# Kernel tuning notes

Measured on AMD Instinct MI355X. Metric: run time of the kernel, lower is better.

The kernel has to match this reference:

```python
import jax, jax.numpy as jnp
import numpy as np

DIM = 96
HEADS = 8
HH = 128
WW = 128
L = HH * WW
K = 256
B = 2


def setup_inputs() -> dict:
    key = jax.random.key(0)
    ks = jax.random.split(key, 8)
    s = 0.02
    return {
        "x": jax.random.normal(ks[0], (B, L, DIM), jnp.float32),
        "Wqkv": jax.random.normal(ks[1], (DIM, 3 * DIM), jnp.float32) * s,
        "W0": jax.random.normal(ks[2], (DIM, DIM), jnp.float32) * s,
        "E": jax.random.normal(ks[3], (L, K), jnp.float32) * s,
        "conv0_w": jax.random.normal(ks[4], (DIM, 1, 5, 5), jnp.float32) * s,
        "conv0_b": jnp.zeros((DIM,), jnp.float32),
        "conv_sp_w": jax.random.normal(ks[5], (DIM, 1, 7, 7), jnp.float32) * s,
        "conv_sp_b": jnp.zeros((DIM,), jnp.float32),
        "conv1_w": jax.random.normal(ks[6], (DIM, DIM, 1, 1), jnp.float32) * s,
        "conv1_b": jnp.zeros((DIM,), jnp.float32),
        "H": HH,
        "W": WW,
    }


def _conv(x, w, b, pad, dil, groups):
    y = jax.lax.conv_general_dilated(
        x, w, window_strides=(1, 1), padding=[(pad, pad), (pad, pad)],
        rhs_dilation=(dil, dil),
        dimension_numbers=("NCHW", "OIHW", "NCHW"),
        feature_group_count=groups)
    return y + b[None, :, None, None]


def _cnn_atten(x, H, W, conv0_w, conv0_b, conv_sp_w, conv_sp_b, conv1_w, conv1_b):
    # VAN-style Large-Kernel-Attention: dw5x5 -> dw7x7(dil=3) -> 1x1, gate by identity
    Bx, Lx, C = x.shape
    xi = x.reshape(Bx, H, W, C).transpose(0, 3, 1, 2)  # B,C,H,W
    a = _conv(xi, conv0_w, conv0_b, 2, 1, C)
    a = _conv(a, conv_sp_w, conv_sp_b, 9, 3, C)
    a = _conv(a, conv1_w, conv1_b, 0, 1, 1)
    out = xi * a
    return out.transpose(0, 2, 3, 1).reshape(Bx, Lx, C)


def reference(x, Wqkv, W0, E, conv0_w, conv0_b, conv_sp_w, conv_sp_b, conv1_w, conv1_b, H, W):
    Bx, Lx, C = x.shape
    dh = C // HEADS
    scale = dh ** (-0.5)
    qkv = (x @ Wqkv).reshape(Bx, Lx, 3, HEADS, dh).transpose(2, 0, 3, 1, 4)  # 3,B,h,L,d
    q, k, v = qkv[0], qkv[1], qkv[2]
    ca = _cnn_atten(x, H, W, conv0_w, conv0_b, conv_sp_w, conv_sp_b, conv1_w, conv1_b)  # B,L,C
    vf = v.transpose(0, 2, 1, 3).reshape(Bx, Lx, C)
    vf = ca * vf  # elementwise CNN gating of V
    v = vf.reshape(Bx, Lx, HEADS, dh).transpose(0, 2, 1, 3)  # B,h,L,d
    # Linformer-style sequence reduction: L -> K
    v = jnp.einsum("bhjd,jk->bhkd", v, E)
    k = jnp.einsum("bhjd,jk->bhkd", k, E)
    attn = jax.nn.softmax(jnp.einsum("bhid,bhkd->bhik", q, k) * scale, axis=-1)  # B,h,L,K
    o = jnp.einsum("bhik,bhkd->bhid", attn, v)
    o = o.transpose(0, 2, 1, 3).reshape(Bx, Lx, C)
    return o @ W0
```

## Files before the change

kernel.cpp:

```cpp
#include <hip/hip_runtime.h>

#define HH_ 128
#define WW_ 128
#define LL_ (HH_*WW_)
#define NH 8
#define DHD 12
#define KD 256
#define BB_ 2
#define NROW (BB_*LL_)

typedef __attribute__((ext_vector_type(8))) short short8v;
typedef __attribute__((ext_vector_type(4))) float f32x4;
typedef unsigned short ushortT;

__device__ __forceinline__ float4 ld4(const float* p) {
    return *reinterpret_cast<const float4*>(p);
}
__device__ __forceinline__ unsigned int pk2(float a, float b) {
    unsigned int ua = __float_as_uint(a);
    unsigned int ub = __float_as_uint(b);
    ua = (ua + 0x7FFFu + ((ua >> 16) & 1u)) >> 16;
    ub = (ub + 0x7FFFu + ((ub >> 16) & 1u)) >> 16;
    return ua | (ub << 16);
}
__device__ __forceinline__ ushortT bf1(float a) {
    unsigned int u = __float_as_uint(a);
    return (ushortT)((u + 0x7FFFu + ((u >> 16) & 1u)) >> 16);
}
__device__ __forceinline__ float ubf(ushortT v) {
    return __uint_as_float(((unsigned int)v) << 16);
}
__device__ __forceinline__ unsigned int cvtpk(float a, float b) {
    unsigned int r;
    asm("v_cvt_pk_bf16_f32 %0, %1, %2" : "=v"(r) : "v"(a), "v"(b));
    return r;
}

__global__ __launch_bounds__(256) void k_front(const float* __restrict__ x,
        const float* __restrict__ c0w, const float* __restrict__ c0b,
        const float* __restrict__ E, const float* __restrict__ Wq,
        const float* __restrict__ W0, const float* __restrict__ w1,
        float* __restrict__ a1, ushortT* __restrict__ ET,
        ushortT* __restrict__ wqT, ushortT* __restrict__ w0T,
        ushortT* __restrict__ w1c) {
    __shared__ __align__(16) float shf[2400];
    const int tid = threadIdx.x;
    if (blockIdx.x < 1024) {
        float* wl = shf;
        for (int i = tid; i < 25*96; i += 256) {
            int c = i / 25, t = i % 25;
            wl[t*96 + c] = c0w[i];
        }
        __syncthreads();
        const int c4 = (tid & 7)*4;
        const int px = tid >> 3;
        const int pix0 = blockIdx.x * 32;
        const int b = pix0 >> 14;
        const int y = (pix0 & 16383) >> 7;
        const int xx = (pix0 & 127) + px;
        float4 acc[3];
#pragma unroll
        for (int ch = 0; ch < 3; ++ch) { acc[ch].x=0.f; acc[ch].y=0.f; acc[ch].z=0.f; acc[ch].w=0.f; }
#pragma unroll
        for (int iy = 0; iy < 5; ++iy) {
            int y2 = y + iy - 2;
            if (y2 < 0 || y2 >= HH_) continue;
#pragma unroll
            for (int ix = 0; ix < 5; ++ix) {
                int x2 = xx + ix - 2;
                if (x2 < 0 || x2 >= WW_) continue;
                const float* src = x + ((b << 14) + y2*WW_ + x2)*96;
                const float* wt = &wl[(iy*5 + ix)*96];
#pragma unroll
                for (int ch = 0; ch < 3; ++ch) {
                    float4 xv = ld4(src + ch*32 + c4);
                    float4 wv = ld4(wt + ch*32 + c4);
                    acc[ch].x = fmaf(xv.x, wv.x, acc[ch].x);
                    acc[ch].y = fmaf(xv.y, wv.y, acc[ch].y);
                    acc[ch].z = fmaf(xv.z, wv.z, acc[ch].z);
                    acc[ch].w = fmaf(xv.w, wv.w, acc[ch].w);
                }
            }
        }
        float* dst = a1 + (long)(pix0 + px)*96;
#pragma unroll
        for (int ch = 0; ch < 3; ++ch) {
            float4 bv = ld4(c0b + ch*32 + c4);
            float4 r;
            r.x = acc[ch].x + bv.x; r.y = acc[ch].y + bv.y;
            r.z = acc[ch].z + bv.z; r.w = acc[ch].w + bv.w;
            *reinterpret_cast<float4*>(dst + ch*32 + c4) = r;
        }
    } else if (blockIdx.x < 2048) {
        ushortT* Tz = (ushortT*)shf;
        const int bid = blockIdx.x - 1024;
        const int jt = bid >> 2, kt = bid & 3;
        const int j0 = jt * 64, kk0 = kt * 64;
        for (int i = tid; i < 64*16; i += 256) {
            int row = i >> 4, s4 = (i & 15) << 2;
            float4 e4 = ld4(&E[(long)(j0 + row)*256 + kk0 + s4]);
            Tz[(s4 + 0)*66 + row] = bf1(e4.x);
            Tz[(s4 + 1)*66 + row] = bf1(e4.y);
            Tz[(s4 + 2)*66 + row] = bf1(e4.z);
            Tz[(s4 + 3)*66 + row] = bf1(e4.w);
        }
        __syncthreads();
        unsigned int* Tu = (unsigned int*)Tz;
        for (int i = tid; i < 64*32; i += 256) {
            int kk = i >> 5, s = i & 31;
            ((unsigned int*)ET)[(((long)(kk0 + kk) << 14) + j0 >> 1) + s] = Tu[kk*33 + s];
        }
    } else {
        int i = (blockIdx.x - 2048)*256 + tid;
        if (i < 27648) {
            int n = i / 96, k = i % 96;
            wqT[n*96 + k] = bf1(Wq[k*288 + n]);
        } else if (i < 36864) {
            int j = i - 27648;
            int n = j / 96, k = j % 96;
            w0T[n*96 + k] = bf1(W0[k*96 + n]);
        } else if (i < 46080) {
            int j = i - 36864;
            w1c[j] = bf1(w1[j]);
        }
    }
}

__global__ __launch_bounds__(256) void k_mid(const float* __restrict__ x,
        const ushortT* __restrict__ wqT, ushortT* __restrict__ qkv16,
        const float* __restrict__ a1, const float* __restrict__ cspw,
        const float* __restrict__ cspb, ushortT* __restrict__ a2_16) {
    __shared__ __align__(16) float shm[4704];
    const int tid = threadIdx.x;
    if (blockIdx.x < 512) {
        ushortT* xb = (ushortT*)shm;
        const int r0w = blockIdx.x * 64;
        for (int i = tid; i < 64*48; i += 256) {
            int r = i / 48, cp = i % 48;
            const float* sp = x + (long)(r0w + r)*96 + cp*2;
            ((unsigned int*)xb)[r*52 + cp] = pk2(sp[0], sp[1]);
        }
        __syncthreads();
        const int lane = tid & 63, wv = tid >> 6;
        const int l15 = lane & 15, l4 = lane >> 4;
        short8v bx[3];
#pragma unroll
        for (int kt = 0; kt < 3; ++kt)
            bx[kt] = *(const short8v*)((const short*)xb + (wv*16 + l15)*104 + kt*32 + l4*8);
#pragma unroll 2
        for (int mt = 0; mt < 18; ++mt) {
            f32x4 acc = {0.f, 0.f, 0.f, 0.f};
#pragma unroll
            for (int kt = 0; kt < 3; ++kt) {
                short8v a = *(const short8v*)((const short*)wqT + (mt*16 + l15)*96 + kt*32 + l4*8);
                acc = __builtin_amdgcn_mfma_f32_16x16x32_bf16(a, bx[kt], acc, 0, 0, 0);
            }
            unsigned int* q32 = (unsigned int*)(qkv16 + (long)(r0w + wv*16 + l15)*288 + mt*16 + l4*4);
            q32[0] = pk2(acc[0], acc[1]);
            q32[1] = pk2(acc[2], acc[3]);
        }
    } else {
        float* wl = shm;
        for (int i = tid; i < 49*96; i += 256) {
            int c = i / 49, t = i % 49;
            wl[t*96 + c] = cspw[i];
        }
        __syncthreads();
        const int c4 = (tid & 7)*4;
        const int px = tid >> 3;
        const int pix0 = (blockIdx.x - 512) * 32;
        const int b = pix0 >> 14;
        const int y = (pix0 & 16383) >> 7;
        const int xx = (pix0 & 127) + px;
        float4 acc[3];
#pragma unroll
        for (int ch = 0; ch < 3; ++ch) { acc[ch].x=0.f; acc[ch].y=0.f; acc[ch].z=0.f; acc[ch].w=0.f; }
#pragma unroll
        for (int iy = 0; iy < 7; ++iy) {
            int y2 = y + iy*3 - 9;
            if (y2 < 0 || y2 >= HH_) continue;
#pragma unroll
            for (int ix = 0; ix < 7; ++ix) {
                int x2 = xx + ix*3 - 9;
                if (x2 < 0 || x2 >= WW_) continue;
                const float* src = a1 + ((b << 14) + y2*WW_ + x2)*96;
                const float* wt = &wl[(iy*7 + ix)*96];
#pragma unroll
                for (int ch = 0; ch < 3; ++ch) {
                    float4 xv = ld4(src + ch*32 + c4);
                    float4 wv = ld4(wt + ch*32 + c4);
                    acc[ch].x = fmaf(xv.x, wv.x, acc[ch].x);
                    acc[ch].y = fmaf(xv.y, wv.y, acc[ch].y);
                    acc[ch].z = fmaf(xv.z, wv.z, acc[ch].z);
                    acc[ch].w = fmaf(xv.w, wv.w, acc[ch].w);
                }
            }
        }
        ushortT* dst = a2_16 + (long)(pix0 + px)*96;
#pragma unroll
        for (int ch = 0; ch < 3; ++ch) {
            float4 bv = ld4(cspb + ch*32 + c4);
            unsigned int* d32 = (unsigned int*)(dst + ch*32 + c4);
            d32[0] = pk2(acc[ch].x + bv.x, acc[ch].y + bv.y);
            d32[1] = pk2(acc[ch].z + bv.z, acc[ch].w + bv.w);
        }
    }
}

__global__ __launch_bounds__(256) void k_pw_gate(const ushortT* __restrict__ a2_16,
        const ushortT* __restrict__ w1c, const float* __restrict__ b1,
        const float* __restrict__ xin, const ushortT* __restrict__ qkv16,
        ushortT* __restrict__ XT) {
    __shared__ ushortT ab[64*104];
    __shared__ ushortT ktile[96*66];
    __shared__ ushortT vtile[96*66];
    const int tid = threadIdx.x;
    const int r0 = blockIdx.x * 64;
    const int b = r0 >> 14, j0 = r0 & 16383;
    const unsigned int* a2u = (const unsigned int*)a2_16;
    for (int i = tid; i < 64*48; i += 256) {
        int r = i / 48, cp = i % 48;
        ((unsigned int*)ab)[r*52 + cp] = a2u[(long)(r0 + r)*48 + cp];
    }
    const unsigned int* q32 = (const unsigned int*)qkv16;
    for (int i = tid; i < 64*48; i += 256) {
        int row = i / 48, cp = i % 48;
        unsigned int kk2 = q32[(long)(r0 + row)*144 + 48 + cp];
        ktile[(2*cp + 0)*66 + row] = (ushortT)(kk2 & 0xFFFF);
        ktile[(2*cp + 1)*66 + row] = (ushortT)(kk2 >> 16);
    }
    __syncthreads();
    const int lane = tid & 63, wv = tid >> 6;
    const int l15 = lane & 15, l4 = lane >> 4;
    const int row = r0 + wv*16 + l15;
    const int jloc = wv*16 + l15;
    short8v bx[3];
#pragma unroll
    for (int kt = 0; kt < 3; ++kt)
        bx[kt] = *(const short8v*)((const short*)ab + (wv*16 + l15)*104 + kt*32 + l4*8);
#pragma unroll
    for (int mt = 0; mt < 6; ++mt) {
        f32x4 acc = {0.f, 0.f, 0.f, 0.f};
#pragma unroll
        for (int kt = 0; kt < 3; ++kt) {
            short8v a = *(const short8v*)((const short*)w1c + (mt*16 + l15)*96 + kt*32 + l4*8);
            acc = __builtin_amdgcn_mfma_f32_16x16x32_bf16(a, bx[kt], acc, 0, 0, 0);
        }
        const int c0 = mt*16 + l4*4;
        float4 b4 = ld4(&b1[c0]);
        float4 x4 = ld4(&xin[(long)row*96 + c0]);
        uint2 vv = *reinterpret_cast<const uint2*>(qkv16 + (long)row*288 + 192 + c0);
        float v0 = ubf((ushortT)(vv.x & 0xFFFF)), v1 = ubf((ushortT)(vv.x >> 16));
        float v2 = ubf((ushortT)(vv.y & 0xFFFF)), v3 = ubf((ushortT)(vv.y >> 16));
        vtile[(c0 + 0)*66 + jloc] = bf1(x4.x * v0 * (acc[0] + b4.x));
        vtile[(c0 + 1)*66 + jloc] = bf1(x4.y * v1 * (acc[1] + b4.y));
        vtile[(c0 + 2)*66 + jloc] = bf1(x4.z * v2 * (acc[2] + b4.z));
        vtile[(c0 + 3)*66 + jloc] = bf1(x4.w * v3 * (acc[3] + b4.w));
    }
    __syncthreads();
    unsigned int* XTu = (unsigned int*)XT;
    unsigned int* ku = (unsigned int*)ktile;
    unsigned int* vu = (unsigned int*)vtile;
    for (int i = tid; i < 96*32; i += 256) {
        int cc = i >> 5, s = i & 31;
        XTu[((((long)b*192 + cc) << 14) + j0 >> 1) + s] = ku[cc*33 + s];
    }
    for (int i = tid; i < 96*32; i += 256) {
        int cc = i >> 5, s = i & 31;
        XTu[((((long)b*192 + 96 + cc) << 14) + j0 >> 1) + s] = vu[cc*33 + s];
    }
}

__global__ __launch_bounds__(512, 2) void k_ered(const ushortT* __restrict__ ET,
        const ushortT* __restrict__ XT, ushortT* __restrict__ part16) {
    const int tid = threadIdx.x;
    const int lane = tid & 63, wv = tid >> 6;
    const int l15 = lane & 15, l4 = lane >> 4;
    const int mtg = wv & 3, nth = wv >> 2;
    const int b  = blockIdx.x >> 7;
    const int jc = blockIdx.x & 127;
    const int j0 = jc * 128;
    f32x4 acc[4][6];
#pragma unroll
    for (int mi = 0; mi < 4; ++mi)
#pragma unroll
        for (int ni = 0; ni < 6; ++ni)
            acc[mi][ni] = (f32x4){0.f, 0.f, 0.f, 0.f};
    const ushortT* Ab = ET + ((long)(mtg*64 + l15) << 14) + j0 + l4*8;
    const ushortT* Bb = XT + (((long)b*192 + nth*96 + l15) << 14) + j0 + l4*8;
#pragma unroll
    for (int ks = 0; ks < 4; ++ks) {
        short8v a[4], bx[6];
#pragma unroll
        for (int mi = 0; mi < 4; ++mi)
            a[mi] = *(const short8v*)(Ab + ((long)mi << 18) + ks*32);
#pragma unroll
        for (int ni = 0; ni < 6; ++ni)
            bx[ni] = *(const short8v*)(Bb + ((long)ni << 18) + ks*32);
#pragma unroll
        for (int mi = 0; mi < 4; ++mi)
#pragma unroll
            for (int ni = 0; ni < 6; ++ni)
                acc[mi][ni] = __builtin_amdgcn_mfma_f32_16x16x32_bf16(a[mi], bx[ni], acc[mi][ni], 0, 0, 0);
    }
    const long base = (long)(b*128 + jc)*49152;
#pragma unroll
    for (int mi = 0; mi < 4; ++mi) {
        int kkb = (mtg*4 + mi)*16 + l4*4;
#pragma unroll
        for (int ni = 0; ni < 6; ++ni) {
            int cc = (nth*6 + ni)*16 + l15;
#pragma unroll
            for (int r = 0; r < 4; ++r)
                part16[base + (long)(kkb + r)*192 + cc] = bf1(acc[mi][ni][r]);
        }
    }
}

__global__ __launch_bounds__(256) void k_ered_fin(const ushortT* __restrict__ part16,
        ushortT* __restrict__ kp16, ushortT* __restrict__ vp16) {
    const int idx = blockIdx.x*256 + threadIdx.x;
    const int c  = idx % 96;
    const int kk = (idx / 96) % 256;
    const int m  = (idx / (96*256)) % 2;
    const int b  = idx / (96*256*2);
    float s = 0.f;
    long off = ((long)(b*128)*256 + kk)*192 + m*96 + c;
    for (int jc = 0; jc < 128; ++jc) {
        s += ubf(part16[off]);
        off += 49152;
    }
    const int h = c / DHD, d = c % DHD;
    if (m == 0) {
        kp16[((b*NH + h)*256 + kk)*16 + d] = bf1(s * 0.4164701998f);
        if (d < 4) kp16[((b*NH + h)*256 + kk)*16 + 12 + d] = 0;
    } else {
        vp16[((b*NH + h)*16 + d)*256 + kk] = bf1(s);
        if (d < 4)
            vp16[((b*NH + h)*16 + 12 + d)*256 + kk] = (d == 0) ? (ushortT)0x3F80 : (ushortT)0;
    }
}

__global__ __launch_bounds__(256, 4) void k_attn(const ushortT* __restrict__ qkv16,
        const ushortT* __restrict__ kp16, const ushortT* __restrict__ vp16,
        ushortT* __restrict__ obuf) {
    __shared__ ushortT lds[24720];
    const int tid = threadIdx.x;
    const int lane = tid & 63, wv = tid >> 6;
    const int l15 = lane & 15, l4 = lane >> 4;
    const int bid = blockIdx.x;
    const int r0 = (bid >> 3) * 64;
    const int h = bid & 7;
    const int b = r0 >> 14;
    {
        const uint4* ksrc = (const uint4*)(kp16 + ((long)(b*NH + h) << 12));
        uint4* kdst = (uint4*)lds;
        kdst[tid] = ksrc[tid];
        kdst[256 + tid] = ksrc[256 + tid];
        const uint4* vsrc = (const uint4*)(vp16 + ((long)(b*NH + h) << 12));
        uint4* vdst = (uint4*)(lds + 4112);
        int r1 = tid >> 5, s1 = tid & 31;
        vdst[r1*33 + s1] = vsrc[tid];
        int j2 = tid + 256;
        int r2 = j2 >> 5, s2 = j2 & 31;
        vdst[r2*33 + s2] = vsrc[j2];
        if (tid < 2) ((uint4*)(lds + 4096))[tid] = (uint4){0u, 0u, 0u, 0u};
    }
    __syncthreads();
    ushortT* Pw = lds + 8336 + wv*4096;
    unsigned int* Pu = (unsigned int*)Pw;
    const int wbase = (l4 >> 1)*64 + l15*4 + (l4 & 1)*2;
    const f32x4 z = {0.f, 0.f, 0.f, 0.f};
    const int row0 = r0 + wv*16;
    short8v bq = {0, 0, 0, 0, 0, 0, 0, 0};
    {
        unsigned int* bq32 = (unsigned int*)&bq;
        const ushortT* qp = qkv16 + (long)(row0 + l15)*288 + h*12;
        if (l4 == 0) {
            uint2 t0 = *reinterpret_cast<const uint2*>(qp);
            uint2 t1 = *reinterpret_cast<const uint2*>(qp + 4);
            bq32[0] = t0.x; bq32[1] = t0.y; bq32[2] = t1.x; bq32[3] = t1.y;
        } else if (l4 == 1) {
            uint2 t0 = *reinterpret_cast<const uint2*>(qp + 8);
            bq32[0] = t0.x; bq32[1] = t0.y;
        }
    }
    const ushortT* kpl = lds + l15*16 + l4*8;
#pragma unroll
    for (int mt = 0; mt < 16; ++mt) {
        short8v a = *(const short8v*)(kpl + mt*256);
        f32x4 s = __builtin_amdgcn_mfma_f32_16x16x32_bf16(a, bq, z, 0, 0, 0);
        unsigned int* dst = Pu + (mt >> 1)*256 + (mt & 1)*128 + wbase;
        dst[0] = cvtpk(exp2f(s[0]), exp2f(s[1]));
        dst[1] = cvtpk(exp2f(s[2]), exp2f(s[3]));
    }
    f32x4 o = z;
    const ushortT* vpl = lds + 4112 + l15*264 + l4*8;
#pragma unroll
    for (int ks = 0; ks < 8; ++ks) {
        short8v bp = *(const short8v*)(Pw + ks*512 + l4*128 + l15*8);
        short8v av = *(const short8v*)(vpl + ks*32);
        o = __builtin_amdgcn_mfma_f32_16x16x32_bf16(av, bp, o, 0, 0, 0);
    }
    float rinv = 1.0f / __shfl(o[0], 48 + l15, 64);
    if (l4 < 3) {
        unsigned int* od = (unsigned int*)(obuf + (long)(row0 + l15)*96 + h*12 + l4*4);
        od[0] = cvtpk(o[0]*rinv, o[1]*rinv);
        od[1] = cvtpk(o[2]*rinv, o[3]*rinv);
    }
}

__global__ __launch_bounds__(256) void k_out(const ushortT* __restrict__ obuf,
        const ushortT* __restrict__ w0T, float* __restrict__ out) {
    __shared__ ushortT ol[64*104];
    const int tid = threadIdx.x;
    const int r0 = blockIdx.x * 64;
    for (int i = tid; i < 768; i += 256) {
        int r = i / 12, sg = i % 12;
        *reinterpret_cast<uint4*>(&ol[r*104 + sg*8]) =
            *reinterpret_cast<const uint4*>(&obuf[(long)(r0 + r)*96 + sg*8]);
    }
    __syncthreads();
    const int lane = tid & 63, wv = tid >> 6;
    const int l15 = lane & 15, l4 = lane >> 4;
    short8v a[3];
#pragma unroll
    for (int kt = 0; kt < 3; ++kt)
        a[kt] = *(const short8v*)((const short*)ol + (wv*16 + l15)*104 + kt*32 + l4*8);
#pragma unroll
    for (int nt = 0; nt < 6; ++nt) {
        f32x4 acc = {0.f, 0.f, 0.f, 0.f};
#pragma unroll
        for (int kt = 0; kt < 3; ++kt) {
            short8v bw = *(const short8v*)((const short*)w0T + (nt*16 + l15)*96 + kt*32 + l4*8);
            acc = __builtin_amdgcn_mfma_f32_16x16x32_bf16(a[kt], bw, acc, 0, 0, 0);
        }
#pragma unroll
        for (int r = 0; r < 4; ++r)
            out[(long)(r0 + wv*16 + l4*4 + r)*96 + nt*16 + l15] = acc[r];
    }
}

extern "C" void kernel_launch(void* const* d_in, const int* in_sizes, int n_in,
                              void* d_out, int out_size, void* d_ws, size_t ws_size,
                              hipStream_t stream) {
    (void)in_sizes; (void)n_in; (void)out_size; (void)ws_size;
    const float* x    = (const float*)d_in[0];
    const float* Wqkv = (const float*)d_in[1];
    const float* W0   = (const float*)d_in[2];
    const float* E    = (const float*)d_in[3];
    const float* c0w  = (const float*)d_in[4];
    const float* c0b  = (const float*)d_in[5];
    const float* cspw = (const float*)d_in[6];
    const float* cspb = (const float*)d_in[7];
    const float* c1w  = (const float*)d_in[8];
    const float* c1b  = (const float*)d_in[9];
    float* out = (float*)d_out;
    float* ws  = (float*)d_ws;

    ushortT* qkv16  = (ushortT*)ws;
    ushortT* wqT16  = (ushortT*)(ws + 4718592);
    ushortT* w0T16  = (ushortT*)(ws + 4732416);
    ushortT* w1c16  = (ushortT*)(ws + 4737024);
    ushortT* ET16   = (ushortT*)(ws + 4741632);
    ushortT* XT16   = (ushortT*)(ws + 6838784);
    float* a1       = ws + 9984512;
    ushortT* a2_16  = (ushortT*)(ws + 13130240);
    ushortT* part16 = (ushortT*)(ws + 9984512);
    ushortT* obuf   = (ushortT*)(ws + 9984512);
    ushortT* kp16   = (ushortT*)(ws + 16275968);
    ushortT* vp16   = (ushortT*)(ws + 16308736);

    k_front<<<dim3(2228), dim3(256), 0, stream>>>(x, c0w, c0b, E, Wqkv, W0, c1w,
                                                  a1, ET16, wqT16, w0T16, w1c16);
    k_mid<<<dim3(1536), dim3(256), 0, stream>>>(x, wqT16, qkv16, a1, cspw, cspb, a2_16);
    k_pw_gate<<<dim3(NROW/64), dim3(256), 0, stream>>>(a2_16, w1c16, c1b, x, qkv16, XT16);
    k_ered<<<dim3(256), dim3(512), 0, stream>>>(ET16, XT16, part16);
    k_ered_fin<<<dim3(384), dim3(256), 0, stream>>>(part16, kp16, vp16);
    k_attn<<<dim3((NROW/64)*NH), dim3(256), 0, stream>>>(qkv16, kp16, vp16, obuf);
    k_out<<<dim3(NROW/64), dim3(256), 0, stream>>>(obuf, w0T16, out);
}
```

Before: 132.2 us.

## Pad dilated-conv intermediate with zero halo and make conv loops branch-free

The 5x5 depthwise conv now writes its output into a buffer padded with a 9-pixel zero border (146x146 per image), and extra blocks in the front kernel zero that border. The dilated 7x7 conv can then read neighbours without bounds checks, batching all loads of a kernel row into registers before the FMAs. The 5x5 conv clamps coordinates and masks the weights instead of branching, and both kernels get a launch-bounds occupancy hint. The cost is a larger workspace, extra writes for the border, and higher register pressure from the preloaded tiles, which may limit occupancy.

```diff
diff --git a/kernel.cpp b/kernel.cpp
--- a/kernel.cpp
+++ b/kernel.cpp
@@ -8,6 +8,8 @@
 #define KD 256
 #define BB_ 2
 #define NROW (BB_*LL_)
+#define PW 146
+#define PPB (PW*PW)
 
 typedef __attribute__((ext_vector_type(8))) short short8v;
 typedef __attribute__((ext_vector_type(4))) float f32x4;
@@ -36,11 +38,11 @@
     return r;
 }
 
-__global__ __launch_bounds__(256) void k_front(const float* __restrict__ x,
+__global__ __launch_bounds__(256, 4) void k_front(const float* __restrict__ x,
         const float* __restrict__ c0w, const float* __restrict__ c0b,
         const float* __restrict__ E, const float* __restrict__ Wq,
         const float* __restrict__ W0, const float* __restrict__ w1,
-        float* __restrict__ a1, ushortT* __restrict__ ET,
+        float* __restrict__ a1p, ushortT* __restrict__ ET,
         ushortT* __restrict__ wqT, ushortT* __restrict__ w0T,
         ushortT* __restrict__ w1c) {
     __shared__ __align__(16) float shf[2400];
@@ -64,25 +66,34 @@
 #pragma unroll
         for (int iy = 0; iy < 5; ++iy) {
             int y2 = y + iy - 2;
-            if (y2 < 0 || y2 >= HH_) continue;
+            int y2c = min(max(y2, 0), 127);
+            float fy = ((unsigned)y2 < 128u) ? 1.f : 0.f;
+            float4 xv[5][3];
 #pragma unroll
             for (int ix = 0; ix < 5; ++ix) {
                 int x2 = xx + ix - 2;
-                if (x2 < 0 || x2 >= WW_) continue;
-                const float* src = x + ((b << 14) + y2*WW_ + x2)*96;
-                const float* wt = &wl[(iy*5 + ix)*96];
+                int x2c = min(max(x2, 0), 127);
+                const float* src = x + ((b << 14) + y2c*WW_ + x2c)*96 + c4;
+#pragma unroll
+                for (int ch = 0; ch < 3; ++ch) xv[ix][ch] = ld4(src + ch*32);
+            }
+#pragma unroll
+            for (int ix = 0; ix < 5; ++ix) {
+                int x2 = xx + ix - 2;
+                float f = fy * (((unsigned)x2 < 128u) ? 1.f : 0.f);
+                const float* wt = &wl[(iy*5 + ix)*96 + c4];
 #pragma unroll
                 for (int ch = 0; ch < 3; ++ch) {
-                    float4 xv = ld4(src + ch*32 + c4);
-                    float4 wv = ld4(wt + ch*32 + c4);
-                    acc[ch].x = fmaf(xv.x, wv.x, acc[ch].x);
-                    acc[ch].y = fmaf(xv.y, wv.y, acc[ch].y);
-                    acc[ch].z = fmaf(xv.z, wv.z, acc[ch].z);
-                    acc[ch].w = fmaf(xv.w, wv.w, acc[ch].w);
+                    float4 wv = ld4(wt + ch*32);
+                    wv.x *= f; wv.y *= f; wv.z *= f; wv.w *= f;
+                    acc[ch].x = fmaf(xv[ix][ch].x, wv.x, acc[ch].x);
+                    acc[ch].y = fmaf(xv[ix][ch].y, wv.y, acc[ch].y);
+                    acc[ch].z = fmaf(xv[ix][ch].z, wv.z, acc[ch].z);
+                    acc[ch].w = fmaf(xv[ix][ch].w, wv.w, acc[ch].w);
                 }
             }
         }
-        float* dst = a1 + (long)(pix0 + px)*96;
+        float* dst = a1p + ((long)b*PPB + (y + 9)*PW + xx + 9)*96;
 #pragma unroll
         for (int ch = 0; ch < 3; ++ch) {
             float4 bv = ld4(c0b + ch*32 + c4);
@@ -110,7 +121,7 @@
             int kk = i >> 5, s = i & 31;
             ((unsigned int*)ET)[(((long)(kk0 + kk) << 14) + j0 >> 1) + s] = Tu[kk*33 + s];
         }
-    } else {
+    } else if (blockIdx.x < 2228) {
         int i = (blockIdx.x - 2048)*256 + tid;
         if (i < 27648) {
             int n = i / 96, k = i % 96;
@@ -123,12 +134,25 @@
             int j = i - 36864;
             w1c[j] = bf1(w1[j]);
         }
-    }
-}
-
-__global__ __launch_bounds__(256) void k_mid(const float* __restrict__ x,
+    } else {
+        int gid = (blockIdx.x - 2228)*256 + tid;
+        if (gid < 9864) {
+            int bb = gid / 4932, hp = gid % 4932;
+            int y, xp;
+            if (hp < 1314)      { y = hp / 146;              xp = hp % 146; }
+            else if (hp < 2628) { int h2 = hp - 1314; y = 137 + h2/146; xp = h2 % 146; }
+            else if (hp < 3780) { int h2 = hp - 2628; y = 9 + h2/9;     xp = h2 % 9; }
+            else                { int h2 = hp - 3780; y = 9 + h2/9;     xp = 137 + h2 % 9; }
+            float4* p = (float4*)(a1p + ((long)bb*PPB + y*PW + xp)*96);
+#pragma unroll
+            for (int t = 0; t < 24; ++t) p[t] = (float4){0.f, 0.f, 0.f, 0.f};
+        }
+    }
+}
+
+__global__ __launch_bounds__(256, 4) void k_mid(const float* __restrict__ x,
         const ushortT* __restrict__ wqT, ushortT* __restrict__ qkv16,
-        const float* __restrict__ a1, const float* __restrict__ cspw,
+        const float* __restrict__ a1p, const float* __restrict__ cspw,
         const float* __restrict__ cspb, ushortT* __restrict__ a2_16) {
     __shared__ __align__(16) float shm[4704];
     const int tid = threadIdx.x;
@@ -172,27 +196,29 @@
         const int b = pix0 >> 14;
         const int y = (pix0 & 16383) >> 7;
         const int xx = (pix0 & 127) + px;
+        const float* base = a1p + ((long)b*PPB + y*PW + xx)*96 + c4;
         float4 acc[3];
 #pragma unroll
         for (int ch = 0; ch < 3; ++ch) { acc[ch].x=0.f; acc[ch].y=0.f; acc[ch].z=0.f; acc[ch].w=0.f; }
 #pragma unroll
         for (int iy = 0; iy < 7; ++iy) {
-            int y2 = y + iy*3 - 9;
-            if (y2 < 0 || y2 >= HH_) continue;
+            const float* rp = base + iy*3*PW*96;
+            float4 xv[7][3];
+#pragma unroll
+            for (int ix = 0; ix < 7; ++ix)
+#pragma unroll
+                for (int ch = 0; ch < 3; ++ch)
+                    xv[ix][ch] = ld4(rp + ix*3*96 + ch*32);
 #pragma unroll
             for (int ix = 0; ix < 7; ++ix) {
-                int x2 = xx + ix*3 - 9;
-                if (x2 < 0 || x2 >= WW_) continue;
-                const float* src = a1 + ((b << 14) + y2*WW_ + x2)*96;
-                const float* wt = &wl[(iy*7 + ix)*96];
+                const float* wt = &wl[(iy*7 + ix)*96 + c4];
 #pragma unroll
                 for (int ch = 0; ch < 3; ++ch) {
-                    float4 xv = ld4(src + ch*32 + c4);
-                    float4 wv = ld4(wt + ch*32 + c4);
-                    acc[ch].x = fmaf(xv.x, wv.x, acc[ch].x);
-                    acc[ch].y = fmaf(xv.y, wv.y, acc[ch].y);
-                    acc[ch].z = fmaf(xv.z, wv.z, acc[ch].z);
-                    acc[ch].w = fmaf(xv.w, wv.w, acc[ch].w);
+                    float4 wv = ld4(wt + ch*32);
+                    acc[ch].x = fmaf(xv[ix][ch].x, wv.x, acc[ch].x);
+                    acc[ch].y = fmaf(xv[ix][ch].y, wv.y, acc[ch].y);
+                    acc[ch].z = fmaf(xv[ix][ch].z, wv.z, acc[ch].z);
+                    acc[ch].w = fmaf(xv[ix][ch].w, wv.w, acc[ch].w);
                 }
             }
         }
@@ -464,16 +490,16 @@
     ushortT* w1c16  = (ushortT*)(ws + 4737024);
     ushortT* ET16   = (ushortT*)(ws + 4741632);
     ushortT* XT16   = (ushortT*)(ws + 6838784);
-    float* a1       = ws + 9984512;
-    ushortT* a2_16  = (ushortT*)(ws + 13130240);
+    float* a1p      = ws + 9984512;
+    ushortT* a2_16  = (ushortT*)(ws + 14077184);
     ushortT* part16 = (ushortT*)(ws + 9984512);
     ushortT* obuf   = (ushortT*)(ws + 9984512);
     ushortT* kp16   = (ushortT*)(ws + 16275968);
     ushortT* vp16   = (ushortT*)(ws + 16308736);
 
-    k_front<<<dim3(2228), dim3(256), 0, stream>>>(x, c0w, c0b, E, Wqkv, W0, c1w,
-                                                  a1, ET16, wqT16, w0T16, w1c16);
-    k_mid<<<dim3(1536), dim3(256), 0, stream>>>(x, wqT16, qkv16, a1, cspw, cspb, a2_16);
+    k_front<<<dim3(2268), dim3(256), 0, stream>>>(x, c0w, c0b, E, Wqkv, W0, c1w,
+                                                  a1p, ET16, wqT16, w0T16, w1c16);
+    k_mid<<<dim3(1536), dim3(256), 0, stream>>>(x, wqT16, qkv16, a1p, cspw, cspb, a2_16);
     k_pw_gate<<<dim3(NROW/64), dim3(256), 0, stream>>>(a2_16, w1c16, c1b, x, qkv16, XT16);
     k_ered<<<dim3(256), dim3(512), 0, stream>>>(ET16, XT16, part16);
     k_ered_fin<<<dim3(384), dim3(256), 0, stream>>>(part16, kp16, vp16);
```

After: 138.9 us. +5.1%, slower.
